# Performance work log

Measured on AMD Instinct MI355X. Metric: run time of the kernel, lower is better.

The kernel has to match this reference:

```python
import jax, jax.numpy as jnp
import numpy as np

T, B, D, N, REL, OUT = 16, 128, 96, 8, 96, 64  # time, batch, slot_size, num_slot, rel_size, out_att_size
EPS = 1e-5


def setup_inputs() -> dict:
    key = jax.random.key(0)
    ks = jax.random.split(key, 12)
    rn = lambda k, shape, s: jax.random.normal(k, shape, dtype=jnp.float32) * s
    stdev_i = 1.0 / np.sqrt(2.0 * D)
    stdev_r = 1.0 / np.sqrt(2.0 * D + N)
    return {
        'x': jax.random.normal(ks[0], (T, B, D), dtype=jnp.float32),
        'Wqkv': rn(ks[1], (D, 3 * N), 0.1), 'bqkv': jnp.zeros((3 * N,), jnp.float32),
        'ln_g': jnp.ones((D, 3 * N), jnp.float32), 'ln_b': jnp.zeros((D, 3 * N), jnp.float32),
        'a1': rn(ks[2], (), 0.1), 'a2': rn(ks[3], (), 0.1), 'a3': rn(ks[4], (), 0.1),
        'W2': rn(ks[5], (N * D, D), 0.03), 'b2': jnp.zeros((D,), jnp.float32),
        'Wr': rn(ks[6], (D * D, REL), 0.01), 'br': jnp.zeros((REL,), jnp.float32),
        'W3': rn(ks[7], (N * REL, OUT), 0.03), 'b3': jnp.zeros((OUT,), jnp.float32),
        'item_bias': jax.random.uniform(ks[8], (D, D), jnp.float32, -stdev_i, stdev_i),
        'rel_bias': jax.random.uniform(ks[9], (N, D, D), jnp.float32, -stdev_r, stdev_r),
    }


def reference(x, Wqkv, bqkv, ln_g, ln_b, a1, a2, a3, W2, b2, Wr, br, W3, b3, item_bias, rel_bias):
    Bb = x.shape[1]
    Mi0 = jnp.broadcast_to(item_bias, (Bb, D, D))
    rel0 = jnp.broadcast_to(rel_bias, (Bb, N, D, D))
    W2r = W2.reshape(N, D, D)  # rel_projector2 weight, rows indexed by flattened (n, d)

    def step(carry, xt):  # xt: [B, D]
        Mi, rel = carry
        Mi = Mi + xt[:, :, None] * xt[:, None, :]                     # Mi + outer(x, x)
        Vtr = jnp.einsum('bdf,bndf->bf', Mi, rel)                     # [B, D]
        X2 = Vtr[:, :, None] * xt[:, None, :]                         # [B, D, D]
        qkv = (Mi + a2 * X2) @ Wqkv + bqkv                            # [B, D, 3N]
        mu = qkv.mean(axis=(1, 2), keepdims=True)                     # LayerNorm over [D, 3N]
        var = qkv.var(axis=(1, 2), keepdims=True)
        qkv = (qkv - mu) * jax.lax.rsqrt(var + EPS) * ln_g + ln_b
        qkv = qkv.transpose(0, 2, 1)                                  # [B, 3N, D]
        q, k, v = qkv[:, :N], qkv[:, N:2 * N], qkv[:, 2 * N:]
        # op_att: out[b,i] = sum_j outer(tanh(q_i * k_j), v_j)
        t = jnp.tanh(q[:, :, None, :] * k[:, None, :, :])             # [B, N, N, D]
        R0 = jnp.einsum('bijd,bje->bide', t, v)                       # [B, N, D, D]
        rel = a1 * rel + R0
        R2 = jnp.einsum('bnde,ndf->bef', R0, W2r) + b2                # [B, D, D]
        Mi = Mi + a3 * R2
        r_vec = (rel.reshape(Bb, N, D * D) @ Wr + br).reshape(Bb, N * REL)
        out = r_vec @ W3 + b3                                          # [B, OUT]
        return (Mi, rel), out

    (_, _), hx = jax.lax.scan(step, (Mi0, rel0), x)
    return hx  # [T, B, OUT]
```

## Files before the change

kernel.cpp:

```cpp
#include <hip/hip_runtime.h>
#include <math.h>

#define T_ 16
#define B_ 128
#define C3 24
#define OUT_ 64
#define EPS_ 1e-5f

typedef __attribute__((ext_vector_type(8))) short bf16x8;
typedef __attribute__((ext_vector_type(4))) float f32x4;

union FragU { unsigned u[4]; bf16x8 f; };

__device__ __forceinline__ short f2bf(float x) {
    unsigned u = __float_as_uint(x);
    return (short)((u + 0x7fffu + ((u >> 16) & 1u)) >> 16);
}
__device__ __forceinline__ void splitf(float x, short& h, short& l) {
    unsigned u = __float_as_uint(x);
    unsigned hb = (u + 0x7fffu + ((u >> 16) & 1u)) & 0xffff0000u;
    float res = x - __uint_as_float(hb);
    unsigned v = __float_as_uint(res);
    h = (short)(hb >> 16);
    l = (short)((v + 0x7fffu + ((v >> 16) & 1u)) >> 16);
}
__device__ __forceinline__ f32x4 mfma16(bf16x8 a, bf16x8 b, f32x4 c) {
    return __builtin_amdgcn_mfma_f32_16x16x32_bf16(a, b, c, 0, 0, 0);
}
__device__ __forceinline__ float fast_tanh(float z) {
    float a = fminf(fabsf(z), 9.0f);
    float e = __expf(2.0f * a);
    float t = 1.0f - 2.0f / (e + 1.0f);
    return copysignf(t, z);
}

__global__ __launch_bounds__(768, 1) void prep_mega(
    const float* __restrict__ Wr, const float* __restrict__ W2, const float* __restrict__ W3,
    const float* __restrict__ rel_bias,
    short* __restrict__ WrBH, short* __restrict__ WrBL,
    short* __restrict__ W2H, short* __restrict__ W2L,
    short* __restrict__ W3H, short* __restrict__ W3L,
    float* __restrict__ y0)
{
    const int bid = blockIdx.x, tid = threadIdx.x;
    if (bid < 1152) {
        int idx = bid * 768 + tid;
        int jj = idx & 7, lane = (idx >> 3) & 63, f = idx >> 9;
        int kf = f % 3, rt = (f / 3) % 6, d = f / 18;
        int col = lane & 15, grp = lane >> 4;
        int e = kf * 32 + grp * 8 + jj;
        int r = rt * 16 + col;
        short h, l; splitf(Wr[(size_t)(d * 96 + e) * 96 + r], h, l);
        WrBH[idx] = h; WrBL[idx] = l;
    } else if (bid < 1248) {
        int idx = (bid - 1152) * 768 + tid;
        int jj = idx & 7, lane = (idx >> 3) & 63, kb = (idx >> 9) % 24, rt = idx / (512 * 24);
        int col = lane & 15, grp = lane >> 4;
        int kp = kb * 32 + grp * 8 + jj;
        int d = kp >> 3, n = kp & 7;
        int f = rt * 16 + col;
        short h, l; splitf(W2[(size_t)(n * 96 + d) * 96 + f], h, l);
        W2H[idx] = h; W2L[idx] = l;
    } else if (bid < 1312) {
        int idx = (bid - 1248) * 768 + tid;
        int jj = idx & 7, lane = (idx >> 3) & 63, kb = (idx >> 9) % 24, ot = idx / (512 * 24);
        int col = lane & 15, grp = lane >> 4;
        int k = kb * 32 + grp * 8 + jj, o = ot * 16 + col;
        short h, l; splitf(W3[(size_t)k * 64 + o], h, l);
        W3H[idx] = h; W3L[idx] = l;
    } else {
        __shared__ float s[768];
        const int blk = bid - 1312;
        const int n = blk >> 3, sl = blk & 7;
        const int r = tid % 96, p = tid / 96;
        const float* rb = rel_bias + n * 9216 + sl * 1152;
        float acc = 0.f;
        for (int i = p * 144; i < p * 144 + 144; ++i)
            acc += rb[i] * Wr[(size_t)(sl * 1152 + i) * 96 + r];
        s[tid] = acc;
        __syncthreads();
        if (tid < 96) {
            float tot = 0.f;
            for (int q = 0; q < 8; ++q) tot += s[q * 96 + tid];
            atomicAdd(&y0[n * 96 + tid], tot);
        }
    }
}

__global__ __attribute__((amdgpu_flat_work_group_size(768, 768), amdgpu_waves_per_eu(3, 3)))
void stm_rec(
    const float* __restrict__ x, const float* __restrict__ Wqkv, const float* __restrict__ bqkv,
    const float* __restrict__ ln_g, const float* __restrict__ ln_b,
    const float* __restrict__ a1p, const float* __restrict__ a2p, const float* __restrict__ a3p,
    const float* __restrict__ b2,
    const float* __restrict__ item_bias, const float* __restrict__ rel_bias,
    const short* __restrict__ W2H, const short* __restrict__ W2L,
    short* __restrict__ t2g, short* __restrict__ vgb)
{
    __shared__ __attribute__((aligned(16))) char smem[102336];
    const int tid = threadIdx.x;
    const int b = blockIdx.x;
    const int wv = tid >> 6, lane = tid & 63, col = lane & 15, grp = lane >> 4;
    const float a1 = a1p[0], a2 = a2p[0], a3 = a3p[0];

    float* s_xall    = (float*)(smem);
    float* s_scr     = (float*)(smem + 6144);
    float* s_scrB    = (float*)(smem + 15360);
    float* s_Wq      = (float*)(smem + 18432);
    float* s_lng     = (float*)(smem + 27648);
    float* s_lnb     = (float*)(smem + 36864);
    float* s_tsum    = (float*)(smem + 46080);
    float* s_v       = (float*)(smem + 49152);
    float* s_G0      = (float*)(smem + 52224);
    float* s_G1      = (float*)(smem + 55296);
    float* s_xtWqAll = (float*)(smem + 58368);
    float* s_b2Wq    = (float*)(smem + 59904);
    float* s_bq      = (float*)(smem + 60000);
    float* s_b2v     = (float*)(smem + 60096);
    float* s_red     = (float*)(smem + 60480);
    short* s_tH      = (short*)(smem + 60608);
    short* s_tL      = (short*)(smem + 73024);
    short* s_t2L     = (short*)(smem + 85440);
    float* s_vp      = (float*)(smem + 97728);

    const int de = tid >> 3, ef0 = (tid & 7) * 12;
    float rMi[12], rS[12], rQ[3];
#pragma unroll
    for (int ii = 0; ii < 12; ++ii) {
        int idx = de * 96 + ef0 + ii;
        rMi[ii] = item_bias[idx];
        float ss = 0.f;
        for (int n = 0; n < 8; ++n) ss += rel_bias[n * 9216 + idx];
        rS[ii] = ss;
    }

    for (int i = tid; i < 1536; i += 768)
        s_xall[i] = x[((size_t)(i / 96) * B_ + b) * 96 + (i % 96)];
    for (int i = tid; i < 2304; i += 768) {
        s_Wq[i] = Wqkv[i]; s_lng[i] = ln_g[i]; s_lnb[i] = ln_b[i];
    }
    if (tid < 24) s_bq[tid] = bqkv[tid];
    if (tid < 96) s_b2v[tid] = b2[tid];
    __syncthreads();
#pragma unroll
    for (int pp = 0; pp < 3; ++pp) {
        int o = tid + 768 * pp; int i = o / C3, c = o % C3;
        float acc = 0.f;
        const float* ib = item_bias + i * 96;
        for (int k = 0; k < 96; ++k) acc += ib[k] * s_Wq[k * C3 + c];
        rQ[pp] = acc;
    }
    { int c = tid % C3, p = tid / C3; float acc = 0.f;
      for (int k = 3 * p; k < 3 * p + 3; ++k) acc += s_b2v[k] * s_Wq[k * C3 + c];
      s_scr[tid] = acc; }
    if (tid < 384) {
        int t = tid / 24, c = tid % 24;
        float acc = 0.f;
        const float* xr = s_xall + t * 96;
        for (int k = 0; k < 96; ++k) acc += xr[k] * s_Wq[k * C3 + c];
        s_xtWqAll[tid] = acc;
    }
    __syncthreads();
    if (tid < C3) { float a = 0.f; for (int p = 0; p < 32; ++p) a += s_scr[p * C3 + tid]; s_b2Wq[tid] = a; }
    __syncthreads();

    for (int t = 0; t < T_; ++t) {
        const float* xt = s_xall + t * 96;
        const float* xtWq = s_xtWqAll + t * 24;
        {
            float xde = xt[de];
            const float4* xp = (const float4*)&xt[ef0];
            float4 x0 = xp[0], x1 = xp[1], x2 = xp[2];
            rMi[0] += xde * x0.x; rMi[1] += xde * x0.y; rMi[2] += xde * x0.z; rMi[3] += xde * x0.w;
            rMi[4] += xde * x1.x; rMi[5] += xde * x1.y; rMi[6] += xde * x1.z; rMi[7] += xde * x1.w;
            rMi[8] += xde * x2.x; rMi[9] += xde * x2.y; rMi[10] += xde * x2.z; rMi[11] += xde * x2.w;
        }
        {
            float p12[12];
#pragma unroll
            for (int ii = 0; ii < 12; ++ii) p12[ii] = rMi[ii] * rS[ii];
#pragma unroll
            for (int ii = 0; ii < 12; ++ii) {
                p12[ii] += __shfl_xor(p12[ii], 8);
                p12[ii] += __shfl_xor(p12[ii], 16);
                p12[ii] += __shfl_xor(p12[ii], 32);
            }
            if ((lane >> 3) == 0) {
#pragma unroll
                for (int ii = 0; ii < 12; ++ii)
                    s_vp[wv * 96 + (lane & 7) * 12 + ii] = p12[ii];
            }
        }
        __syncthreads();
        {
            const int i0 = tid / 24, c = tid % 24;
            float ls = 0.f, lq = 0.f;
#pragma unroll
            for (int pp = 0; pp < 3; ++pp) {
                const int i = i0 + 32 * pp;
                float vtr = 0.f;
#pragma unroll
                for (int w = 0; w < 12; ++w) vtr += s_vp[w * 96 + i];
                rQ[pp] += xt[i] * xtWq[c];
                float qv = rQ[pp] + a2 * vtr * xtWq[c] + s_bq[c];
                s_scr[tid + 768 * pp] = qv;
                ls += qv; lq += qv * qv;
            }
            for (int off = 32; off > 0; off >>= 1) { ls += __shfl_down(ls, off); lq += __shfl_down(lq, off); }
            if (lane == 0) { s_red[wv] = ls; s_red[16 + wv] = lq; }
        }
        __syncthreads();
        {
            float S = 0.f, Qs = 0.f;
            for (int w = 0; w < 12; ++w) { S += s_red[w]; Qs += s_red[16 + w]; }
            const float mu = S * (1.0f / 2304.f);
            const float rstd = rsqrtf(Qs * (1.0f / 2304.f) - mu * mu + EPS_);
            const int j = tid / 96, d = tid % 96;
            {
                int o = d * C3 + 16 + j;
                float vv = (s_scr[o] - mu) * rstd * s_lng[o] + s_lnb[o];
                s_v[tid] = vv;
                vgb[((size_t)(t * B_ + b)) * 768 + tid] = f2bf(vv);
            }
            int ok = d * C3 + 8 + j;
            float kk = (s_scr[ok] - mu) * rstd * s_lng[ok] + s_lnb[ok];
            float tv0, tv1;
            unsigned hp0, hp1, hp2, hp3, lp0, lp1, lp2, lp3;
            float ts = 0.f;
#pragma unroll
            for (int q = 0; q < 4; ++q) {
                int oq0 = d * C3 + 2 * q, oq1 = oq0 + 1;
                float q0 = (s_scr[oq0] - mu) * rstd * s_lng[oq0] + s_lnb[oq0];
                float q1 = (s_scr[oq1] - mu) * rstd * s_lng[oq1] + s_lnb[oq1];
                tv0 = fast_tanh(q0 * kk);
                tv1 = fast_tanh(q1 * kk);
                ts += tv0 + tv1;
                short h0, l0, h1, l1;
                splitf(tv0, h0, l0); splitf(tv1, h1, l1);
                unsigned hh = (unsigned)(unsigned short)h0 | ((unsigned)(unsigned short)h1 << 16);
                unsigned ll = (unsigned)(unsigned short)l0 | ((unsigned)(unsigned short)l1 << 16);
                if (q == 0) { hp0 = hh; lp0 = ll; }
                else if (q == 1) { hp1 = hh; lp1 = ll; }
                else if (q == 2) { hp2 = hh; lp2 = ll; }
                else { hp3 = hh; lp3 = ll; }
                s_t2L[(2 * q) * 768 + d * 8 + j] = h0;
                s_t2L[(2 * q + 1) * 768 + d * 8 + j] = h1;
            }
            *(uint4*)&s_tH[j * 776 + d * 8] = make_uint4(hp0, hp1, hp2, hp3);
            *(uint4*)&s_tL[j * 776 + d * 8] = make_uint4(lp0, lp1, lp2, lp3);
            s_tsum[j * 96 + d] = ts;
        }
        __syncthreads();
        *(uint4*)&t2g[((size_t)(t * B_ + b)) * 6144 + tid * 8] = *(const uint4*)&s_t2L[tid * 8];
        {
            const int rt = wv % 6, kh = wv / 6;
            f32x4 aHH = {0,0,0,0}, aLH = {0,0,0,0}, aHL = {0,0,0,0}, aLL = {0,0,0,0};
#pragma unroll 4
            for (int s2 = 0; s2 < 12; ++s2) {
                int kb = kh * 12 + s2;
                bf16x8 ah = {}; bf16x8 al = {};
                if (col < 8) {
                    ah = *(const bf16x8*)&s_tH[col * 776 + kb * 32 + grp * 8];
                    al = *(const bf16x8*)&s_tL[col * 776 + kb * 32 + grp * 8];
                }
                int fo = ((rt * 24 + kb) * 64 + lane) * 8;
                bf16x8 bh = *(const bf16x8*)&W2H[fo];
                bf16x8 bl = *(const bf16x8*)&W2L[fo];
                aHH = mfma16(ah, bh, aHH);
                aLH = mfma16(al, bh, aLH);
                aHL = mfma16(ah, bl, aHL);
                aLL = mfma16(al, bl, aLL);
            }
            f32x4 accG;
#pragma unroll
            for (int reg = 0; reg < 4; ++reg) accG[reg] = (aHH[reg] + aLH[reg]) + (aHL[reg] + aLL[reg]);
            float* dst = (kh == 0) ? s_G0 : s_G1;
            if (grp < 2) {
#pragma unroll
                for (int reg = 0; reg < 4; ++reg)
                    dst[(grp * 4 + reg) * 96 + rt * 16 + col] = accG[reg];
            }
        }
        __syncthreads();
        { int oo = tid % 192, q = tid / 192; int jg = oo / C3, cc = oo % C3;
          float a = 0.f;
          for (int f = q * 24; f < q * 24 + 24; ++f)
              a += (s_G0[jg * 96 + f] + s_G1[jg * 96 + f]) * s_Wq[f * C3 + cc];
          s_scrB[tid] = a; }
        {
            float sn[12], r2[12];
#pragma unroll
            for (int ii = 0; ii < 12; ++ii) { sn[ii] = 0.f; r2[ii] = 0.f; }
#pragma unroll
            for (int j = 0; j < 8; ++j) {
                const float tj = s_tsum[j * 96 + de];
                const float vj = s_v[j * 96 + de];
                const float4* vp = (const float4*)&s_v[j * 96 + ef0];
                const float4* g0 = (const float4*)&s_G0[j * 96 + ef0];
                const float4* g1 = (const float4*)&s_G1[j * 96 + ef0];
#pragma unroll
                for (int q4 = 0; q4 < 3; ++q4) {
                    float4 vv = vp[q4], ga = g0[q4], gb = g1[q4];
                    float gx = ga.x + gb.x, gy = ga.y + gb.y, gz = ga.z + gb.z, gw = ga.w + gb.w;
                    sn[q4*4+0] += tj*vv.x; sn[q4*4+1] += tj*vv.y;
                    sn[q4*4+2] += tj*vv.z; sn[q4*4+3] += tj*vv.w;
                    r2[q4*4+0] += vj*gx; r2[q4*4+1] += vj*gy;
                    r2[q4*4+2] += vj*gz; r2[q4*4+3] += vj*gw;
                }
            }
#pragma unroll
            for (int ii = 0; ii < 12; ++ii) {
                rS[ii] = a1 * rS[ii] + sn[ii];
                rMi[ii] += a3 * (r2[ii] + s_b2v[ef0 + ii]);
            }
        }
        __syncthreads();
#pragma unroll
        for (int pp = 0; pp < 3; ++pp) {
            int o = tid + 768 * pp; int i = o / C3, c = o % C3;
            float a = s_b2Wq[c];
#pragma unroll
            for (int j = 0; j < 8; ++j) {
                float g = s_scrB[j * C3 + c] + s_scrB[192 + j * C3 + c]
                        + s_scrB[384 + j * C3 + c] + s_scrB[576 + j * C3 + c];
                a += s_v[j * 96 + i] * g;
            }
            rQ[pp] += a3 * a;
        }
    }
}

__global__ __launch_bounds__(384, 2) void stm_tail(
    const short* __restrict__ WrBH, const short* __restrict__ WrBL,
    const short* __restrict__ W3H, const short* __restrict__ W3L,
    const short* __restrict__ t2g, const short* __restrict__ vgb,
    float* __restrict__ zg)
{
    __shared__ __attribute__((aligned(16))) short sPT[6 * 5120];
    short* DyH = sPT;
    short* DyL = sPT + 6208;

    const int tid = threadIdx.x;
    const int b = blockIdx.x >> 1, tg = blockIdx.x & 1;
    const int wv6 = tid >> 6, lane = tid & 63, col = lane & 15, grp = lane >> 4;
    const int rt6 = wv6;
    const int th = tg * 8;
    short* PTw = sPT + wv6 * 5120;

    bf16x8 Av[4][3];
#pragma unroll
    for (int p = 0; p < 4; ++p)
#pragma unroll
        for (int kf = 0; kf < 3; ++kf) {
            int t = th + 2 * p + (col >> 3);
            int j = col & 7;
            uint4 z = *(const uint4*)&vgb[((size_t)(t * B_ + b)) * 768 + j * 96 + kf * 32 + grp * 8];
            FragU F; F.u[0] = z.x; F.u[1] = z.y; F.u[2] = z.z; F.u[3] = z.w;
            Av[p][kf] = F.f;
        }
    f32x4 accD[8];
#pragma unroll
    for (int btl = 0; btl < 8; ++btl) accD[btl] = (f32x4){0.f, 0.f, 0.f, 0.f};

    FragU A2r[8];
    bf16x8 bhA[3], blA[3], bhB[3], blB[3];
#pragma unroll
    for (int kf = 0; kf < 3; ++kf) {
        const int fo = ((0 * 18 + rt6 * 3 + kf) * 64 + lane) * 8;
        bhA[kf] = *(const bf16x8*)&WrBH[fo];
        blA[kf] = *(const bf16x8*)&WrBL[fo];
    }

#define TAIL_BODY(DL, CH, CL, NH, NL)                                          \
    {                                                                          \
        const int d = g4 * 4 + (DL);                                           \
        if ((DL) < 3 || g4 < 23) {                                             \
            const int dn = d + 1;                                              \
            _Pragma("unroll")                                                  \
            for (int kf = 0; kf < 3; ++kf) {                                   \
                const int fo = ((dn * 18 + rt6 * 3 + kf) * 64 + lane) * 8;     \
                NH[kf] = *(const bf16x8*)&WrBH[fo];                            \
                NL[kf] = *(const bf16x8*)&WrBL[fo];                            \
            }                                                                  \
        }                                                                      \
        if ((DL) == 1) {                                                       \
            _Pragma("unroll")                                                  \
            for (int btl = 0; btl < 8; ++btl) {                                \
                A2r[btl].u[0] = 0; A2r[btl].u[1] = 0;                          \
                A2r[btl].u[2] = 0; A2r[btl].u[3] = 0;                          \
                if (col < 8) {                                                 \
                    const int tt = th + btl;                                   \
                    uint4 z = *(const uint4*)&t2g[((size_t)(tt * B_ + b)) * 6144 \
                              + col * 768 + g4 * 32 + grp * 8];                \
                    A2r[btl].u[0] = z.x; A2r[btl].u[1] = z.y;                  \
                    A2r[btl].u[2] = z.z; A2r[btl].u[3] = z.w;                  \
                }                                                              \
            }                                                                  \
        }                                                                      \
        f32x4 aPv[4];                                                          \
        _Pragma("unroll")                                                      \
        for (int p = 0; p < 4; ++p) aPv[p] = (f32x4){0.f, 0.f, 0.f, 0.f};      \
        _Pragma("unroll")                                                      \
        for (int kf = 0; kf < 3; ++kf) {                                       \
            _Pragma("unroll")                                                  \
            for (int p = 0; p < 4; ++p) aPv[p] = mfma16(Av[p][kf], CH[kf], aPv[p]); \
            _Pragma("unroll")                                                  \
            for (int p = 0; p < 4; ++p) aPv[p] = mfma16(Av[p][kf], CL[kf], aPv[p]); \
        }                                                                      \
        {                                                                      \
            const int j0 = (grp & 1) * 4;                                      \
            const int bo = grp >> 1;                                           \
            _Pragma("unroll")                                                  \
            for (int p = 0; p < 4; ++p) {                                      \
                const int btl = 2 * p + bo;                                    \
                uint2 uu;                                                      \
                uu.x = (unsigned)(unsigned short)f2bf(aPv[p][0]) |             \
                       ((unsigned)(unsigned short)f2bf(aPv[p][1]) << 16);      \
                uu.y = (unsigned)(unsigned short)f2bf(aPv[p][2]) |             \
                       ((unsigned)(unsigned short)f2bf(aPv[p][3]) << 16);      \
                *(uint2*)&PTw[btl * 640 + col * 40 + (DL) * 8 + j0] = uu;      \
            }                                                                  \
        }                                                                      \
        if ((DL) == 3) {                                                       \
            _Pragma("unroll")                                                  \
            for (int btl = 0; btl < 8; ++btl) {                                \
                bf16x8 B2 = *(const bf16x8*)&PTw[btl * 640 + col * 40 + grp * 8]; \
                accD[btl] = mfma16(A2r[btl].f, B2, accD[btl]);                 \
            }                                                                  \
        }                                                                      \
    }

    for (int g4 = 0; g4 < 24; ++g4) {
        TAIL_BODY(0, bhA, blA, bhB, blB)
        TAIL_BODY(1, bhB, blB, bhA, blA)
        TAIL_BODY(2, bhA, blA, bhB, blB)
        TAIL_BODY(3, bhB, blB, bhA, blA)
    }
#undef TAIL_BODY

    __syncthreads();
    if (grp < 2) {
#pragma unroll
        for (int btl = 0; btl < 8; ++btl)
#pragma unroll
            for (int reg = 0; reg < 4; ++reg) {
                short h, l; splitf(accD[btl][reg], h, l);
                int idx = btl * 776 + (grp * 4 + reg) * 96 + rt6 * 16 + col;
                DyH[idx] = h; DyL[idx] = l;
            }
    }
    __syncthreads();
    if (wv6 < 4) {
        const int ot = wv6;
        f32x4 zHH = {0,0,0,0}, zLH = {0,0,0,0}, zHL = {0,0,0,0};
#pragma unroll 4
        for (int kb = 0; kb < 24; ++kb) {
            bf16x8 ah = {}; bf16x8 al = {};
            if (col < 8) {
                ah = *(const bf16x8*)&DyH[col * 776 + kb * 32 + grp * 8];
                al = *(const bf16x8*)&DyL[col * 776 + kb * 32 + grp * 8];
            }
            int fo = ((ot * 24 + kb) * 64 + lane) * 8;
            bf16x8 bhw = *(const bf16x8*)&W3H[fo];
            bf16x8 blw = *(const bf16x8*)&W3L[fo];
            zHH = mfma16(ah, bhw, zHH);
            zLH = mfma16(al, bhw, zLH);
            zHL = mfma16(ah, blw, zHL);
        }
        if (grp < 2) {
#pragma unroll
            for (int reg = 0; reg < 4; ++reg) {
                int tl = grp * 4 + reg;
                zg[((size_t)(b * 16 + th + tl)) * 64 + ot * 16 + col] = zHH[reg] + zLH[reg] + zHL[reg];
            }
        }
    }
}

__global__ __launch_bounds__(256) void stm_fin(
    const float* __restrict__ W3, const float* __restrict__ b3,
    const float* __restrict__ br, const float* __restrict__ y0,
    const float* __restrict__ a1p, const float* __restrict__ zg,
    float* __restrict__ out)
{
    __shared__ float scanA[256];
    __shared__ float scanB[256];
    const int tid = threadIdx.x, b = blockIdx.x;
    const float a1 = a1p[0];
    {
        const int o = tid & 63, seg = tid >> 6;
        float pa = 0.f, pb = 0.f;
        for (int i = seg * 192; i < seg * 192 + 192; ++i) {
            float w = W3[(size_t)i * 64 + o];
            pa += y0[i] * w;
            pb += br[i % 96] * w;
        }
        scanA[tid] = pa; scanB[tid] = pb;
    }
    __syncthreads();
    if (tid < 64) {
        float c0 = 0.f, cbr = b3[tid];
        for (int s = 0; s < 4; ++s) { c0 += scanA[s * 64 + tid]; cbr += scanB[s * 64 + tid]; }
        float u = c0;
        for (int t = 0; t < T_; ++t) {
            u = a1 * u + zg[((size_t)(b * 16 + t)) * 64 + tid];
            out[((size_t)(t * B_ + b)) * OUT_ + tid] = u + cbr;
        }
    }
}

extern "C" void kernel_launch(void* const* d_in, const int* in_sizes, int n_in,
                              void* d_out, int out_size, void* d_ws, size_t ws_size,
                              hipStream_t stream) {
    const float* x         = (const float*)d_in[0];
    const float* Wqkv      = (const float*)d_in[1];
    const float* bqkv      = (const float*)d_in[2];
    const float* ln_g      = (const float*)d_in[3];
    const float* ln_b      = (const float*)d_in[4];
    const float* a1        = (const float*)d_in[5];
    const float* a2        = (const float*)d_in[6];
    const float* a3        = (const float*)d_in[7];
    const float* W2        = (const float*)d_in[8];
    const float* b2        = (const float*)d_in[9];
    const float* Wr        = (const float*)d_in[10];
    const float* br        = (const float*)d_in[11];
    const float* W3        = (const float*)d_in[12];
    const float* b3        = (const float*)d_in[13];
    const float* item_bias = (const float*)d_in[14];
    const float* rel_bias  = (const float*)d_in[15];
    float* out = (float*)d_out;

    char* ws = (char*)d_ws;
    short* WrBH = (short*)ws;
    short* WrBL = (short*)(ws + 1769472);
    short* W2H  = (short*)(ws + 3538944);
    short* W2L  = (short*)(ws + 3686400);
    short* W3H  = (short*)(ws + 3833856);
    short* W3L  = (short*)(ws + 3932160);
    float* y0   = (float*)(ws + 4030464);
    short* t2g  = (short*)(ws + 4034048);
    short* vgb  = (short*)(ws + 29199872);
    float* zg   = (float*)(ws + 32345600);

    hipMemsetAsync(y0, 0, 3072, stream);
    hipLaunchKernelGGL(prep_mega, dim3(1376), dim3(768), 0, stream,
                       Wr, W2, W3, rel_bias, WrBH, WrBL, W2H, W2L, W3H, W3L, y0);
    hipLaunchKernelGGL(stm_rec, dim3(B_), dim3(768), 0, stream,
                       x, Wqkv, bqkv, ln_g, ln_b, a1, a2, a3,
                       b2, item_bias, rel_bias, W2H, W2L, t2g, vgb);
    hipLaunchKernelGGL(stm_tail, dim3(2 * B_), dim3(384), 0, stream,
                       WrBH, WrBL, W3H, W3L, t2g, vgb, zg);
    hipLaunchKernelGGL(stm_fin, dim3(B_), dim3(256), 0, stream,
                       W3, b3, br, y0, a1, zg, out);
}
```

Measured before the change: 494.1 us.

## Hoist W3 constant reductions into extra tail blocks and use inline-asm MFMA

The per-batch recomputation of the y0·W3 and br·W3 reductions in the final kernel is moved into two extra blocks of the tail kernel, so they run once and write small constant vectors. The final kernel becomes a 64-thread scan that only reads those vectors and zg. The W2 MFMA loop in the recurrent kernel now uses inline-asm MFMA instructions with an explicit nop fence before the accumulators are read, which aims to let the instructions issue back to back. The asm path depends on the manual nop counts being enough for the hardware hazard, and the tail grid's block-index mapping changes.

After: 493.5 us. Within noise of the previous version (-0.1%).

```diff
diff --git a/kernel.cpp b/kernel.cpp
--- a/kernel.cpp
+++ b/kernel.cpp
@@ -27,6 +27,16 @@
 __device__ __forceinline__ f32x4 mfma16(bf16x8 a, bf16x8 b, f32x4 c) {
     return __builtin_amdgcn_mfma_f32_16x16x32_bf16(a, b, c, 0, 0, 0);
 }
+__device__ __forceinline__ f32x4 mfma16v(bf16x8 a, bf16x8 b, f32x4 c) {
+    f32x4 d;
+    asm("s_nop 1\n\tv_mfma_f32_16x16x32_bf16 %0, %1, %2, %3"
+        : "=v"(d)
+        : "v"(a), "v"(b), "0"(c));
+    return d;
+}
+#define MFMA_FENCE4(a0, a1, a2, a3) \
+    asm volatile("s_nop 7\n\ts_nop 7" : "+v"(a0), "+v"(a1), "+v"(a2), "+v"(a3))
+
 __device__ __forceinline__ float fast_tanh(float z) {
     float a = fminf(fabsf(z), 9.0f);
     float e = __expf(2.0f * a);
@@ -266,11 +276,12 @@
                 int fo = ((rt * 24 + kb) * 64 + lane) * 8;
                 bf16x8 bh = *(const bf16x8*)&W2H[fo];
                 bf16x8 bl = *(const bf16x8*)&W2L[fo];
-                aHH = mfma16(ah, bh, aHH);
-                aLH = mfma16(al, bh, aLH);
-                aHL = mfma16(ah, bl, aHL);
-                aLL = mfma16(al, bl, aLL);
-            }
+                aHH = mfma16v(ah, bh, aHH);
+                aLH = mfma16v(al, bh, aLH);
+                aHL = mfma16v(ah, bl, aHL);
+                aLL = mfma16v(al, bl, aLL);
+            }
+            MFMA_FENCE4(aHH, aLH, aHL, aLL);
             f32x4 accG;
 #pragma unroll
             for (int reg = 0; reg < 4; ++reg) accG[reg] = (aHH[reg] + aLH[reg]) + (aHL[reg] + aLL[reg]);
@@ -334,14 +345,46 @@
     const short* __restrict__ WrBH, const short* __restrict__ WrBL,
     const short* __restrict__ W3H, const short* __restrict__ W3L,
     const short* __restrict__ t2g, const short* __restrict__ vgb,
-    float* __restrict__ zg)
+    const float* __restrict__ y0, const float* __restrict__ br,
+    const float* __restrict__ W3f, const float* __restrict__ b3,
+    float* __restrict__ zg, float* __restrict__ c0v, float* __restrict__ cbrv)
 {
     __shared__ __attribute__((aligned(16))) short sPT[6 * 5120];
     short* DyH = sPT;
     short* DyL = sPT + 6208;
 
     const int tid = threadIdx.x;
-    const int b = blockIdx.x >> 1, tg = blockIdx.x & 1;
+
+    if (blockIdx.x >= 256) {
+        float* red = (float*)sPT;
+        const int o = tid & 63, seg = tid >> 6;
+        if (blockIdx.x == 256) {
+            float pa = 0.f;
+            for (int i = seg * 128; i < seg * 128 + 128; ++i)
+                pa += y0[i] * W3f[(size_t)i * 64 + o];
+            red[seg * 64 + o] = pa;
+            __syncthreads();
+            if (tid < 64) {
+                float s = 0.f;
+                for (int q = 0; q < 6; ++q) s += red[q * 64 + tid];
+                c0v[tid] = s;
+            }
+        } else {
+            float pb = 0.f;
+            for (int i = seg * 128; i < seg * 128 + 128; ++i)
+                pb += br[i % 96] * W3f[(size_t)i * 64 + o];
+            red[seg * 64 + o] = pb;
+            __syncthreads();
+            if (tid < 64) {
+                float s = b3[tid];
+                for (int q = 0; q < 6; ++q) s += red[q * 64 + tid];
+                cbrv[tid] = s;
+            }
+        }
+        return;
+    }
+
+    const int b = blockIdx.x & 127, tg = blockIdx.x >> 7;
     const int wv6 = tid >> 6, lane = tid & 63, col = lane & 15, grp = lane >> 4;
     const int rt6 = wv6;
     const int th = tg * 8;
@@ -477,35 +520,18 @@
     }
 }
 
-__global__ __launch_bounds__(256) void stm_fin(
-    const float* __restrict__ W3, const float* __restrict__ b3,
-    const float* __restrict__ br, const float* __restrict__ y0,
+__global__ __launch_bounds__(64) void stm_fin(
     const float* __restrict__ a1p, const float* __restrict__ zg,
+    const float* __restrict__ c0v, const float* __restrict__ cbrv,
     float* __restrict__ out)
 {
-    __shared__ float scanA[256];
-    __shared__ float scanB[256];
     const int tid = threadIdx.x, b = blockIdx.x;
     const float a1 = a1p[0];
-    {
-        const int o = tid & 63, seg = tid >> 6;
-        float pa = 0.f, pb = 0.f;
-        for (int i = seg * 192; i < seg * 192 + 192; ++i) {
-            float w = W3[(size_t)i * 64 + o];
-            pa += y0[i] * w;
-            pb += br[i % 96] * w;
-        }
-        scanA[tid] = pa; scanB[tid] = pb;
-    }
-    __syncthreads();
-    if (tid < 64) {
-        float c0 = 0.f, cbr = b3[tid];
-        for (int s = 0; s < 4; ++s) { c0 += scanA[s * 64 + tid]; cbr += scanB[s * 64 + tid]; }
-        float u = c0;
-        for (int t = 0; t < T_; ++t) {
-            u = a1 * u + zg[((size_t)(b * 16 + t)) * 64 + tid];
-            out[((size_t)(t * B_ + b)) * OUT_ + tid] = u + cbr;
-        }
+    float u = c0v[tid];
+    const float cbr = cbrv[tid];
+    for (int t = 0; t < T_; ++t) {
+        u = a1 * u + zg[((size_t)(b * 16 + t)) * 64 + tid];
+        out[((size_t)(t * B_ + b)) * OUT_ + tid] = u + cbr;
     }
 }
 
@@ -541,6 +567,8 @@
     short* t2g  = (short*)(ws + 4034048);
     short* vgb  = (short*)(ws + 29199872);
     float* zg   = (float*)(ws + 32345600);
+    float* c0v  = (float*)(ws + 32869888);
+    float* cbrv = (float*)(ws + 32870144);
 
     hipMemsetAsync(y0, 0, 3072, stream);
     hipLaunchKernelGGL(prep_mega, dim3(1376), dim3(768), 0, stream,
@@ -548,8 +576,9 @@
     hipLaunchKernelGGL(stm_rec, dim3(B_), dim3(768), 0, stream,
                        x, Wqkv, bqkv, ln_g, ln_b, a1, a2, a3,
                        b2, item_bias, rel_bias, W2H, W2L, t2g, vgb);
-    hipLaunchKernelGGL(stm_tail, dim3(2 * B_), dim3(384), 0, stream,
-                       WrBH, WrBL, W3H, W3L, t2g, vgb, zg);
-    hipLaunchKernelGGL(stm_fin, dim3(B_), dim3(256), 0, stream,
-                       W3, b3, br, y0, a1, zg, out);
-}
+    hipLaunchKernelGGL(stm_tail, dim3(258), dim3(384), 0, stream,
+                       WrBH, WrBL, W3H, W3L, t2g, vgb,
+                       y0, br, W3, b3, zg, c0v, cbrv);
+    hipLaunchKernelGGL(stm_fin, dim3(B_), dim3(64), 0, stream,
+                       a1, zg, c0v, cbrv, out);
+}
```
